# Performance work log

Measured on AMD Instinct MI355X. Metric: run time of the kernel, lower is better.

Reference implementation:

```python
import jax, jax.numpy as jnp
import numpy as np

H = 16  # n_heads


def _ln(x, g, b, eps=1e-5):
    m = x.mean(-1, keepdims=True)
    v = ((x - m) ** 2).mean(-1, keepdims=True)
    return (x - m) / jnp.sqrt(v + eps) * g + b


def setup_inputs() -> dict:
    key = jax.random.key(0)
    ks = jax.random.split(key, 10)
    b, lq, d, dff, L = 2, 1024, 1024, 4096, 4
    s = 0.02
    return {
        "x": jax.random.normal(ks[0], (b, lq, d), jnp.float32),
        "memory_bank": jax.random.normal(ks[1], (L, b, lq, d), jnp.float32),
        "attn_mask": jax.random.bernoulli(ks[2], 0.3, (b, lq, lq)),
        "ln1_g": jnp.ones((d,), jnp.float32),
        "ln1_b": jnp.zeros((d,), jnp.float32),
        "Wq": jax.random.normal(ks[3], (d, d), jnp.float32) * s,
        "Wk": jax.random.normal(ks[4], (d, d), jnp.float32) * s,
        "Wv": jax.random.normal(ks[5], (d, d), jnp.float32) * s,
        "Wo": jax.random.normal(ks[6], (d, d), jnp.float32) * s,
        "ln2_g": jnp.ones((d,), jnp.float32),
        "ln2_b": jnp.zeros((d,), jnp.float32),
        "W1": jax.random.normal(ks[7], (d, dff), jnp.float32) * s,
        "b1": jnp.zeros((dff,), jnp.float32),
        "W2": jax.random.normal(ks[8], (dff, d), jnp.float32) * s,
        "b2": jnp.zeros((d,), jnp.float32),
    }


def reference(x, memory_bank, attn_mask, ln1_g, ln1_b, Wq, Wk, Wv, Wo,
              ln2_g, ln2_b, W1, b1, W2, b2):
    # x: [b, lq, d]; memory_bank: [L, b, lk, d]; attn_mask: [b, lq, lk] bool (True = masked)
    b, lq, d = x.shape
    dh = d // H
    # preprocess_attn: LayerNorm (eval mode -> dropouts are identity)
    q = _ln(x, ln1_g, ln1_b)
    # grow memory bank with current normalized input
    mem = jnp.concatenate([memory_bank, q[None]], axis=0)  # [L+1, b, lk, d]
    L, _, lk, _ = mem.shape
    # projections (bias-free); key/value projected per layer then flattened over (L, lk)
    pq = (q @ Wq).reshape(b, lq, H, dh).transpose(0, 2, 1, 3) * (dh ** -0.5)  # [b,h,lq,dh]
    pk = (mem @ Wk).transpose(1, 0, 2, 3).reshape(b, L * lk, H, dh).transpose(0, 2, 1, 3)
    pv = (mem @ Wv).transpose(1, 0, 2, 3).reshape(b, L * lk, H, dh).transpose(0, 2, 1, 3)
    scores = jnp.einsum('bhqd,bhkd->bhqk', pq, pk)           # [b,h,lq,L*lk]
    scores = scores.reshape(b, H, lq, L, lk)
    scores = jnp.where(attn_mask[:, None, :, None, :], -jnp.inf, scores)
    attn = jax.nn.softmax(scores.reshape(b, H, lq, L * lk), axis=-1)
    ctx = jnp.einsum('bhqk,bhkd->bhqd', attn, pv)            # [b,h,lq,dh]
    ctx = ctx.transpose(0, 2, 1, 3).reshape(b, lq, d)
    attn_out = ctx @ Wo
    # postprocess_attn: residual add
    x2 = x + attn_out
    # FFN: LayerNorm -> Linear -> ReLU -> Linear -> residual
    f = _ln(x2, ln2_g, ln2_b)
    f = jax.nn.relu(f @ W1 + b1) @ W2 + b2
    out = x2 + f
    return (out, mem)
```

## Files before the change

### kernel.cpp

```cpp
#include <hip/hip_runtime.h>
#include <hip/hip_bf16.h>

typedef __attribute__((ext_vector_type(8))) __bf16 bf16x8;
typedef __attribute__((ext_vector_type(4))) __bf16 bf16x4;
typedef __attribute__((ext_vector_type(4))) float f32x4;
typedef __attribute__((ext_vector_type(16))) float f32x16;

#define MFMA16(a, b, c) __builtin_amdgcn_mfma_f32_16x16x32_bf16((a), (b), (c), 0, 0, 0)
#define MFMA32(a, b, c) __builtin_amdgcn_mfma_f32_32x32x16_bf16((a), (b), (c), 0, 0, 0)
#define LOG2E 1.4426950408889634f

static __device__ __forceinline__ float exp2_fast(float x) {
    float r; asm("v_exp_f32 %0, %1" : "=v"(r) : "v"(x)); return r;
}

__device__ __forceinline__ void gll16(const void* g, void* l) {
    __builtin_amdgcn_global_load_lds((const __attribute__((address_space(1))) void*)g,
                                     (__attribute__((address_space(3))) void*)l,
                                     16, 0, 0);
}

__global__ __launch_bounds__(256) void prep_kernel(const float* __restrict__ bank,
                                                   float* __restrict__ mem_out,
                                                   __bf16* __restrict__ membf,
                                                   const float* __restrict__ x,
                                                   const float* __restrict__ g,
                                                   const float* __restrict__ bta,
                                                   float* __restrict__ q_out,
                                                   __bf16* __restrict__ qbf) {
    __shared__ float rs[4], rs2[4];
    int blk = blockIdx.x;
    if (blk < 2048) {
        int i = blk * 256 + threadIdx.x;
        const float4* i4 = (const float4*)bank;
        float4* o4 = (float4*)mem_out;
        for (; i < 2097152; i += 2048 * 256) {
            float4 v = i4[i];
            o4[i] = v;
            if (membf) {
                bf16x4 ob = {(__bf16)v.x, (__bf16)v.y, (__bf16)v.z, (__bf16)v.w};
                ((bf16x4*)membf)[i] = ob;
            }
        }
    } else {
        int row = blk - 2048;
        const float4 v = ((const float4*)(x + (size_t)row * 1024))[threadIdx.x];
        float s = v.x + v.y + v.z + v.w;
        float s2 = v.x * v.x + v.y * v.y + v.z * v.z + v.w * v.w;
#pragma unroll
        for (int off = 1; off < 64; off <<= 1) {
            s += __shfl_xor(s, off);
            s2 += __shfl_xor(s2, off);
        }
        int wv = threadIdx.x >> 6;
        if ((threadIdx.x & 63) == 0) { rs[wv] = s; rs2[wv] = s2; }
        __syncthreads();
        s = rs[0] + rs[1] + rs[2] + rs[3];
        s2 = rs2[0] + rs2[1] + rs2[2] + rs2[3];
        float mean = s * (1.0f / 1024.0f);
        float var = s2 * (1.0f / 1024.0f) - mean * mean;
        float rstd = rsqrtf(var + 1e-5f);
        float4 gg = ((const float4*)g)[threadIdx.x];
        float4 bb = ((const float4*)bta)[threadIdx.x];
        float4 o;
        o.x = (v.x - mean) * rstd * gg.x + bb.x;
        o.y = (v.y - mean) * rstd * gg.y + bb.y;
        o.z = (v.z - mean) * rstd * gg.z + bb.z;
        o.w = (v.w - mean) * rstd * gg.w + bb.w;
        ((float4*)(q_out + (size_t)row * 1024))[threadIdx.x] = o;
        if (qbf) {
            bf16x4 ob = {(__bf16)o.x, (__bf16)o.y, (__bf16)o.z, (__bf16)o.w};
            ((bf16x4*)(qbf + (size_t)row * 1024))[threadIdx.x] = ob;
        }
    }
}

__global__ __launch_bounds__(256) void ln_kernel(const float* __restrict__ x,
                                                 const float* __restrict__ g,
                                                 const float* __restrict__ bta,
                                                 __bf16* __restrict__ outb) {
    int row = blockIdx.x;
    const float4 v = ((const float4*)(x + (size_t)row * 1024))[threadIdx.x];
    float s = v.x + v.y + v.z + v.w;
    float s2 = v.x * v.x + v.y * v.y + v.z * v.z + v.w * v.w;
#pragma unroll
    for (int off = 1; off < 64; off <<= 1) {
        s += __shfl_xor(s, off);
        s2 += __shfl_xor(s2, off);
    }
    __shared__ float rs[4], rs2[4];
    int wv = threadIdx.x >> 6;
    if ((threadIdx.x & 63) == 0) { rs[wv] = s; rs2[wv] = s2; }
    __syncthreads();
    s = rs[0] + rs[1] + rs[2] + rs[3];
    s2 = rs2[0] + rs2[1] + rs2[2] + rs2[3];
    float mean = s * (1.0f / 1024.0f);
    float var = s2 * (1.0f / 1024.0f) - mean * mean;
    float rstd = rsqrtf(var + 1e-5f);
    float4 gg = ((const float4*)g)[threadIdx.x];
    float4 bb = ((const float4*)bta)[threadIdx.x];
    bf16x4 ob;
    ob[0] = (__bf16)((v.x - mean) * rstd * gg.x + bb.x);
    ob[1] = (__bf16)((v.y - mean) * rstd * gg.y + bb.y);
    ob[2] = (__bf16)((v.z - mean) * rstd * gg.z + bb.z);
    ob[3] = (__bf16)((v.w - mean) * rstd * gg.w + bb.w);
    ((bf16x4*)(outb + (size_t)row * 1024))[threadIdx.x] = ob;
}

__global__ __launch_bounds__(256) void comb_ln2(const float* __restrict__ pc0,
                                                const float* __restrict__ pc1,
                                                const float* __restrict__ x,
                                                const float* __restrict__ g,
                                                const float* __restrict__ bta,
                                                float* __restrict__ x2,
                                                __bf16* __restrict__ fln) {
    int row = blockIdx.x;
    int idx = row * 256 + threadIdx.x;
    float4 a = ((const float4*)pc0)[idx];
    float4 b = ((const float4*)pc1)[idx];
    float4 r = ((const float4*)x)[idx];
    float4 v;
    v.x = a.x + b.x + r.x;
    v.y = a.y + b.y + r.y;
    v.z = a.z + b.z + r.z;
    v.w = a.w + b.w + r.w;
    ((float4*)x2)[idx] = v;
    float s = v.x + v.y + v.z + v.w;
    float s2 = v.x * v.x + v.y * v.y + v.z * v.z + v.w * v.w;
#pragma unroll
    for (int off = 1; off < 64; off <<= 1) {
        s += __shfl_xor(s, off);
        s2 += __shfl_xor(s2, off);
    }
    __shared__ float rs[4], rs2[4];
    int wv = threadIdx.x >> 6;
    if ((threadIdx.x & 63) == 0) { rs[wv] = s; rs2[wv] = s2; }
    __syncthreads();
    s = rs[0] + rs[1] + rs[2] + rs[3];
    s2 = rs2[0] + rs2[1] + rs2[2] + rs2[3];
    float mean = s * (1.0f / 1024.0f);
    float var = s2 * (1.0f / 1024.0f) - mean * mean;
    float rstd = rsqrtf(var + 1e-5f);
    float4 gg = ((const float4*)g)[threadIdx.x];
    float4 bb = ((const float4*)bta)[threadIdx.x];
    bf16x4 ob;
    ob[0] = (__bf16)((v.x - mean) * rstd * gg.x + bb.x);
    ob[1] = (__bf16)((v.y - mean) * rstd * gg.y + bb.y);
    ob[2] = (__bf16)((v.z - mean) * rstd * gg.z + bb.z);
    ob[3] = (__bf16)((v.w - mean) * rstd * gg.w + bb.w);
    ((bf16x4*)(fln + (size_t)row * 1024))[threadIdx.x] = ob;
}

__device__ __forceinline__ void tr_body(const float* __restrict__ in, __bf16* __restrict__ out,
                                        int K, int N, int k0, int n0) {
    __shared__ float tile[32][33];
    int tx = threadIdx.x & 31, ty = threadIdx.x >> 5;
#pragma unroll
    for (int i = 0; i < 4; i++)
        tile[ty + i * 8][tx] = in[(size_t)(k0 + ty + i * 8) * N + n0 + tx];
    __syncthreads();
#pragma unroll
    for (int i = 0; i < 4; i++)
        out[(size_t)(n0 + ty + i * 8) * K + k0 + tx] = (__bf16)tile[tx][ty + i * 8];
}

__global__ __launch_bounds__(256) void tr_early(const float* __restrict__ Wq,
                                                const float* __restrict__ Wk,
                                                const float* __restrict__ Wv,
                                                __bf16* __restrict__ Wq_t,
                                                __bf16* __restrict__ Wkv_t) {
    int w = blockIdx.x;
    int sel = w >> 10, within = w & 1023;
    const float* in = (sel == 0) ? Wq : ((sel == 1) ? Wk : Wv);
    __bf16* out = (sel == 0) ? Wq_t : (Wkv_t + (size_t)(sel - 1) * 1048576);
    tr_body(in, out, 1024, 1024, (within >> 5) * 32, (within & 31) * 32);
}

__global__ __launch_bounds__(256) void tr_late(const float* __restrict__ Wo,
                                               const float* __restrict__ W1,
                                               const float* __restrict__ W2,
                                               __bf16* __restrict__ Wo_t,
                                               __bf16* __restrict__ W1_t,
                                               __bf16* __restrict__ W2_t) {
    int w = blockIdx.x;
    const float* in;
    __bf16* out;
    int K, N, k0, n0;
    if (w < 1024) {
        in = Wo; out = Wo_t; K = 1024; N = 1024; n0 = (w & 31) * 32; k0 = (w >> 5) * 32;
    } else if (w < 5120) {
        int v = w - 1024;
        in = W1; out = W1_t; K = 1024; N = 4096; n0 = (v & 127) * 32; k0 = (v >> 7) * 32;
    } else {
        int v = w - 5120;
        in = W2; out = W2_t; K = 4096; N = 1024; n0 = (v & 31) * 32; k0 = (v >> 5) * 32;
    }
    tr_body(in, out, K, N, k0, n0);
}

template <int EPI, bool ABF16>
__device__ __forceinline__ void gemm_core(const void* __restrict__ Av,
                                          const __bf16* __restrict__ Bt,
                                          void* __restrict__ Cout,
                                          const float* __restrict__ bias,
                                          const float* __restrict__ res,
                                          int N, int lda, int ldb, int klen,
                                          float scale, int bm, int bn) {
    constexpr int LDA = ABF16 ? 32 : 40;
    __shared__ __bf16 As[128 * LDA];
    __shared__ __bf16 Bs[128 * 32];

    int t = threadIdx.x;
    int lane = t & 63, wave = t >> 6;
    int wm = (wave >> 1) * 64, wn = (wave & 1) * 64;
    int l16 = lane & 15, l4 = lane >> 4;

    f32x4 acc[4][4];
#pragma unroll
    for (int m = 0; m < 4; m++)
#pragma unroll
        for (int n = 0; n < 4; n++) acc[m][n] = (f32x4){0.f, 0.f, 0.f, 0.f};

    int srow = t >> 2;
    int scol = (t & 3) * 8;
    int ar = t >> 1, ak = (t & 1) * 16;
    const __bf16* Ab = (const __bf16*)Av;
    const float* Af = (const float*)Av;

    for (int k0 = 0; k0 < klen; k0 += 32) {
        gll16(Bt + (size_t)(bn + srow) * ldb + (k0 + scol), &Bs[wave * 512]);
        gll16(Bt + (size_t)(bn + 64 + srow) * ldb + (k0 + scol), &Bs[2048 + wave * 512]);
        if constexpr (ABF16) {
            gll16(Ab + (size_t)(bm + srow) * lda + (k0 + scol), &As[wave * 512]);
            gll16(Ab + (size_t)(bm + 64 + srow) * lda + (k0 + scol), &As[2048 + wave * 512]);
        } else {
            const float* ap = Af + (size_t)(bm + ar) * lda + k0 + ak;
            float4 f0 = ((const float4*)ap)[0];
            float4 f1 = ((const float4*)ap)[1];
            float4 f2 = ((const float4*)ap)[2];
            float4 f3 = ((const float4*)ap)[3];
            float ta[16] = {f0.x, f0.y, f0.z, f0.w, f1.x, f1.y, f1.z, f1.w,
                            f2.x, f2.y, f2.z, f2.w, f3.x, f3.y, f3.z, f3.w};
            bf16x8 v0, v1;
#pragma unroll
            for (int j = 0; j < 8; j++) { v0[j] = (__bf16)ta[j]; v1[j] = (__bf16)ta[j + 8]; }
            *(bf16x8*)&As[ar * 40 + ak] = v0;
            *(bf16x8*)&As[ar * 40 + ak + 8] = v1;
        }
        __syncthreads();

        bf16x8 af[4], bfr[4];
#pragma unroll
        for (int m = 0; m < 4; m++) af[m] = *(const bf16x8*)&As[(wm + m * 16 + l16) * LDA + l4 * 8];
#pragma unroll
        for (int n = 0; n < 4; n++) bfr[n] = *(const bf16x8*)&Bs[(wn + n * 16 + l16) * 32 + l4 * 8];
#pragma unroll
        for (int m = 0; m < 4; m++)
#pragma unroll
            for (int n = 0; n < 4; n++) acc[m][n] = MFMA16(af[m], bfr[n], acc[m][n]);
        __syncthreads();
    }

#pragma unroll
    for (int m = 0; m < 4; m++) {
#pragma unroll
        for (int r = 0; r < 4; r++) {
            int row = bm + wm + m * 16 + l4 * 4 + r;
#pragma unroll
            for (int n = 0; n < 4; n++) {
                int col = bn + wn + n * 16 + l16;
                float c = acc[m][n][r];
                size_t idx = (size_t)row * N + col;
                if (EPI == 0) {
                    ((__bf16*)Cout)[idx] = (__bf16)(c * scale);
                } else if (EPI == 1) {
                    ((float*)Cout)[idx] = c + res[idx];
                } else if (EPI == 2) {
                    ((__bf16*)Cout)[idx] = (__bf16)fmaxf(c + bias[col], 0.0f);
                } else if (EPI == 3) {
                    ((float*)Cout)[idx] = c + bias[col] + res[idx];
                } else {
                    ((float*)Cout)[idx] = c;
                }
            }
        }
    }
}

template <int EPI, bool ABF16>
__global__ __launch_bounds__(256) void gemm_bt(const void* __restrict__ Av,
                                               const __bf16* __restrict__ Bt,
                                               void* __restrict__ Cout,
                                               const float* __restrict__ bias,
                                               const float* __restrict__ res,
                                               int N, int K, float scale, int nbx) {
    int q = gridDim.x >> 3;
    int swz = (blockIdx.x & 7) * q + (blockIdx.x >> 3);
    int bn = (swz % nbx) * 128;
    int bm = (swz / nbx) * 128;
    gemm_core<EPI, ABF16>(Av, Bt, Cout, bias, res, N, K, K, K, scale, bm, bn);
}

template <bool ABF16>
__global__ __launch_bounds__(256) void gemm_proj(const void* __restrict__ Akv,
                                                 const __bf16* __restrict__ Wkv_t,
                                                 __bf16* __restrict__ PKV,
                                                 const void* __restrict__ Aq,
                                                 const __bf16* __restrict__ Wq_t,
                                                 __bf16* __restrict__ Pq) {
    int q = gridDim.x >> 3;
    int swz = (blockIdx.x & 7) * q + (blockIdx.x >> 3);
    const void* A;
    const __bf16* B;
    __bf16* C;
    int N, bm, bn;
    float sc;
    if (swz < 1280) {
        A = Akv; B = Wkv_t; C = PKV; N = 2048; sc = 1.0f;
        bn = (swz & 15) * 128; bm = (swz >> 4) * 128;
    } else {
        int p = swz - 1280;
        A = Aq; B = Wq_t; C = Pq; N = 1024; sc = 0.125f * LOG2E;
        bn = (p & 7) * 128; bm = (p >> 3) * 128;
    }
    gemm_core<0, ABF16>(A, B, C, nullptr, nullptr, N, 1024, 1024, 1024, sc, bm, bn);
}

__global__ __launch_bounds__(256) void gemm_w2(const __bf16* __restrict__ h1,
                                               const __bf16* __restrict__ W2_t,
                                               float* __restrict__ pc0,
                                               float* __restrict__ pc1) {
    int q = gridDim.x >> 3;
    int swz = (blockIdx.x & 7) * q + (blockIdx.x >> 3);
    int half = swz >> 7;
    int p = swz & 127;
    int bn = (p & 7) * 128, bm = (p >> 3) * 128;
    int koff = half * 2048;
    gemm_core<4, true>(h1 + koff, W2_t + koff, half ? pc1 : pc0, nullptr, nullptr,
                       1024, 4096, 4096, 2048, 1.0f, bm, bn);
}

__global__ __launch_bounds__(256) void gemm_wo(const __bf16* __restrict__ ctx,
                                               const __bf16* __restrict__ Wo_t,
                                               float* __restrict__ pc0,
                                               float* __restrict__ pc1) {
    int q = gridDim.x >> 3;
    int swz = (blockIdx.x & 7) * q + (blockIdx.x >> 3);
    int half = swz >> 7;
    int p = swz & 127;
    int bn = (p & 7) * 128, bm = (p >> 3) * 128;
    int koff = half * 512;
    gemm_core<4, true>(ctx + koff, Wo_t + koff, half ? pc1 : pc0, nullptr, nullptr,
                       1024, 1024, 1024, 512, 1.0f, bm, bn);
}

__global__ __launch_bounds__(256) void comb_kernel(const float* __restrict__ pc0,
                                                   const float* __restrict__ pc1,
                                                   const float* __restrict__ bias,
                                                   const float* __restrict__ res,
                                                   float* __restrict__ out) {
    int i = blockIdx.x * 256 + threadIdx.x;
    float4 a = ((const float4*)pc0)[i];
    float4 b = ((const float4*)pc1)[i];
    float4 r = ((const float4*)res)[i];
    float4 o;
    o.x = a.x + b.x + r.x;
    o.y = a.y + b.y + r.y;
    o.z = a.z + b.z + r.z;
    o.w = a.w + b.w + r.w;
    if (bias) {
        float4 bb = ((const float4*)bias)[i & 255];
        o.x += bb.x; o.y += bb.y; o.z += bb.z; o.w += bb.w;
    }
    ((float4*)out)[i] = o;
}

__global__ __launch_bounds__(256, 3) void attn_part(const __bf16* __restrict__ Pq,
                                                    const __bf16* __restrict__ PKV,
                                                    const unsigned char* __restrict__ mask,
                                                    __bf16* __restrict__ pacc,
                                                    float* __restrict__ pl) {
    int bh = blockIdx.x;
    int b = bh >> 4, h = bh & 15;
    int rng = blockIdx.z;
    int wave = threadIdx.x >> 6, lane = threadIdx.x & 63;
    int l32 = lane & 31, hi = lane >> 5;
    int q0 = blockIdx.y * 128 + wave * 32;

    __shared__ __bf16 Ks[64][64];
    __shared__ __bf16 Vt[64][64];
    __shared__ __bf16 Ps[4][32][64];

    bf16x8 qf[4];
    {
        const __bf16* pqrow = Pq + (size_t)(b * 1024 + q0 + l32) * 1024 + h * 64 + hi * 8;
#pragma unroll
        for (int ds = 0; ds < 4; ds++) qf[ds] = *(const bf16x8*)(pqrow + ds * 16);
    }

    f32x16 acc0, acc1;
#pragma unroll
    for (int i = 0; i < 16; i++) { acc0[i] = 0.f; acc1[i] = 0.f; }
    float lsum = 0.0f;

    const unsigned char* mrow_p = mask + (size_t)b * (1024u * 1024u)
                                  + (size_t)(q0 + l32) * 1024 + hi * 4;

    int tl = threadIdx.x;
    int skey = tl >> 2;
    int sd0 = (tl & 3) << 4;
    int kgbase = rng * 1280;

    int Gq = (l32 ^ (l32 >> 3)) & 7;
    int Gk = (skey ^ (skey >> 3)) & 7;
    int kw0 = skey * 64 + ((((sd0 >> 3) + 0) ^ Gk) << 3);
    int kw1 = skey * 64 + ((((sd0 >> 3) + 1) ^ Gk) << 3);
    int vwa[16];
#pragma unroll
    for (int j = 0; j < 16; j++) {
        int row = sd0 + j;
        int Gr = (row ^ (row >> 3)) & 7;
        vwa[j] = row * 64 + ((((skey >> 3) ^ Gr) << 3) | (skey & 7));
    }
    __bf16* KsF = &Ks[0][0];
    __bf16* VtF = &Vt[0][0];
    __bf16* PsF = &Ps[wave][0][0];

    bf16x8 rk0, rk1, rv0, rv1;
    unsigned int mk[8], mkn[8];
    {
        int kg = kgbase + skey;
        int lidx = kg >> 10, i = kg & 1023;
        size_t off = ((size_t)(lidx * 2048 + b * 1024 + i) << 11) + h * 64 + sd0;
        rk0 = *(const bf16x8*)(PKV + off);
        rk1 = *(const bf16x8*)(PKV + off + 8);
        rv0 = *(const bf16x8*)(PKV + off + 1024);
        rv1 = *(const bf16x8*)(PKV + off + 1032);
        int kloc = kgbase & 1023;
#pragma unroll
        for (int d = 0; d < 8; d++)
            mk[d] = *(const unsigned int*)(mrow_p + kloc + (d >> 2) * 32 + (d & 3) * 8);
    }

    for (int t = 0; t < 20; t++) {
        *(bf16x8*)&KsF[kw0] = rk0;
        *(bf16x8*)&KsF[kw1] = rk1;
#pragma unroll
        for (int j = 0; j < 8; j++) { VtF[vwa[j]] = rv0[j]; VtF[vwa[j + 8]] = rv1[j]; }
        __syncthreads();

        if (t + 1 < 20) {
            int kg = kgbase + (t + 1) * 64 + skey;
            int lidx = kg >> 10, i = kg & 1023;
            size_t off = ((size_t)(lidx * 2048 + b * 1024 + i) << 11) + h * 64 + sd0;
            rk0 = *(const bf16x8*)(PKV + off);
            rk1 = *(const bf16x8*)(PKV + off + 8);
            rv0 = *(const bf16x8*)(PKV + off + 1024);
            rv1 = *(const bf16x8*)(PKV + off + 1032);
            int kloc = (kgbase + (t + 1) * 64) & 1023;
#pragma unroll
            for (int d = 0; d < 8; d++)
                mkn[d] = *(const unsigned int*)(mrow_p + kloc + (d >> 2) * 32 + (d & 3) * 8);
        }

        float psum = 0.0f;
#pragma unroll
        for (int kb = 0; kb < 2; kb++) {
            f32x16 s;
#pragma unroll
            for (int i = 0; i < 16; i++) s[i] = 0.f;
            __builtin_amdgcn_s_setprio(1);
#pragma unroll
            for (int ds = 0; ds < 4; ds++) {
                int row = kb * 32 + l32;
                int Gr = (row ^ (row >> 3)) & 7;
                bf16x8 ka = *(const bf16x8*)&KsF[row * 64 + (((ds * 2 + hi) ^ Gr) << 3)];
                s = MFMA32(ka, qf[ds], s);
            }
            __builtin_amdgcn_s_setprio(0);
#pragma unroll
            for (int g = 0; g < 4; g++) {
                bf16x4 pk_;
                unsigned int mkd = mk[kb * 4 + g];
#pragma unroll
                for (int m = 0; m < 4; m++) {
                    float e = exp2_fast(s[g * 4 + m]);
                    e = ((mkd >> (m * 8)) & 255u) ? 0.0f : e;
                    psum += e;
                    pk_[m] = (__bf16)e;
                }
                *(bf16x4*)&PsF[l32 * 64 + ((((kb * 4 + g) ^ Gq) << 3) | (hi * 4))] = pk_;
            }
        }
        lsum += psum;
#pragma unroll
        for (int d = 0; d < 8; d++) mk[d] = mkn[d];

        __builtin_amdgcn_s_setprio(1);
#pragma unroll
        for (int ks = 0; ks < 4; ks++) {
            bf16x8 pf = *(const bf16x8*)&PsF[l32 * 64 + (((ks * 2 + hi) ^ Gq) << 3)];
            {
                int row = l32;
                int Gr = (row ^ (row >> 3)) & 7;
                bf16x8 vf = *(const bf16x8*)&VtF[row * 64 + (((ks * 2 + hi) ^ Gr) << 3)];
                acc0 = MFMA32(vf, pf, acc0);
            }
            {
                int row = 32 + l32;
                int Gr = (row ^ (row >> 3)) & 7;
                bf16x8 vf = *(const bf16x8*)&VtF[row * 64 + (((ks * 2 + hi) ^ Gr) << 3)];
                acc1 = MFMA32(vf, pf, acc1);
            }
        }
        __builtin_amdgcn_s_setprio(0);
        __syncthreads();
    }

    lsum += __shfl_xor(lsum, 32);

    size_t blk = ((size_t)(bh * 8 + blockIdx.y) * 4 + rng);
    __bf16* pa = pacc + blk * 8192 + (size_t)(wave * 32 + l32) * 64;
#pragma unroll
    for (int g = 0; g < 4; g++) {
        bf16x4 o0, o1;
#pragma unroll
        for (int m = 0; m < 4; m++) {
            o0[m] = (__bf16)acc0[g * 4 + m];
            o1[m] = (__bf16)acc1[g * 4 + m];
        }
        *(bf16x4*)&pa[g * 8 + hi * 4] = o0;
        *(bf16x4*)&pa[32 + g * 8 + hi * 4] = o1;
    }
    if (hi == 0) pl[blk * 128 + wave * 32 + l32] = lsum;
}

__global__ __launch_bounds__(512) void attn_comb(const __bf16* __restrict__ pacc,
                                                 const float* __restrict__ pl,
                                                 __bf16* __restrict__ ctx) {
    int bh = blockIdx.x, qb = blockIdx.y;
    int b = bh >> 4, h = bh & 15;
    int q = threadIdx.x >> 2, d0 = (threadIdx.x & 3) * 16;
    float acc[16];
#pragma unroll
    for (int j = 0; j < 16; j++) acc[j] = 0.0f;
    float l = 0.0f;
    size_t blk0 = ((size_t)(bh * 8 + qb)) * 4;
#pragma unroll
    for (int rng = 0; rng < 4; rng++) {
        size_t base = (blk0 + rng) * 8192 + (size_t)q * 64 + d0;
        bf16x8 a0 = *(const bf16x8*)&pacc[base];
        bf16x8 a1 = *(const bf16x8*)&pacc[base + 8];
#pragma unroll
        for (int j = 0; j < 8; j++) {
            acc[j] += (float)a0[j];
            acc[8 + j] += (float)a1[j];
        }
        l += pl[(blk0 + rng) * 128 + q];
    }
    float inv = 1.0f / l;
    __bf16* crow = ctx + ((size_t)(b * 1024 + qb * 128 + q) << 10) + h * 64 + d0;
    bf16x8 o0, o1;
#pragma unroll
    for (int j = 0; j < 8; j++) {
        o0[j] = (__bf16)(acc[j] * inv);
        o1[j] = (__bf16)(acc[8 + j] * inv);
    }
    *(bf16x8*)crow = o0;
    *(bf16x8*)(crow + 8) = o1;
}

#define KHALF 2560
#define CK 64
#define NCH 40
__global__ __launch_bounds__(512, 4) void attn_kernel(const __bf16* __restrict__ Pq,
                                                      const __bf16* __restrict__ PKV,
                                                      const unsigned char* __restrict__ mask,
                                                      __bf16* __restrict__ ctx) {
    int bh = blockIdx.x;
    int b = bh >> 4, h = bh & 15;
    int wave = threadIdx.x >> 6, lane = threadIdx.x & 63;
    int grp = wave >> 2, wv = wave & 3;
    int l16 = lane & 15, l4 = lane >> 4;
    int q0 = blockIdx.y * 64 + wv * 16;

    __shared__ __bf16 Ks[2][64][72];
    __shared__ __bf16 Vt[2][64][72];
    __shared__ __bf16 Ps[8][16][72];

    const f32x4 fzero = {0.f, 0.f, 0.f, 0.f};

    bf16x8 qf[2];
    {
        const __bf16* pqrow = Pq + (size_t)(b * 1024 + q0 + l16) * 1024 + h * 64;
        qf[0] = *(const bf16x8*)(pqrow + l4 * 8);
        qf[1] = *(const bf16x8*)(pqrow + 32 + l4 * 8);
    }

    f32x4 accT[4];
#pragma unroll
    for (int n = 0; n < 4; n++) accT[n] = fzero;
    float lsum = 0.0f;

    const unsigned char* mrow_p = mask + (size_t)b * (1024u * 1024u) + (size_t)(q0 + l16) * 1024;

    int tl = threadIdx.x & 255;
    int skey = tl >> 2;
    int sd0 = (tl & 3) << 4;
    int kgbase = grp * KHALF;

    bf16x8 rk0, rk1, rv0, rv1;
    unsigned int mk[4], mkn[4];
    {
        int kg = kgbase + skey;
        int lidx = kg >> 10, i = kg & 1023;
        size_t off = ((size_t)(lidx * 2048 + b * 1024 + i) << 11) + h * 64 + sd0;
        rk0 = *(const bf16x8*)(PKV + off);
        rk1 = *(const bf16x8*)(PKV + off + 8);
        rv0 = *(const bf16x8*)(PKV + off + 1024);
        rv1 = *(const bf16x8*)(PKV + off + 1032);
        int kloc = kgbase & 1023;
#pragma unroll
        for (int tile = 0; tile < 4; tile++)
            mk[tile] = *(const unsigned int*)(mrow_p + kloc + tile * 16 + l4 * 4);
    }

    for (int t = 0; t < NCH; t++) {
        *(bf16x8*)&Ks[grp][skey][sd0] = rk0;
        *(bf16x8*)&Ks[grp][skey][sd0 + 8] = rk1;
#pragma unroll
        for (int j = 0; j < 8; j++) {
            int row = sd0 + j;
            Vt[grp][row][skey ^ ((row >> 3) << 3)] = rv0[j];
            int row2 = sd0 + 8 + j;
            Vt[grp][row2][skey ^ ((row2 >> 3) << 3)] = rv1[j];
        }
        __syncthreads();

        if (t + 1 < NCH) {
            int kg = kgbase + (t + 1) * CK + skey;
            int lidx = kg >> 10, i = kg & 1023;
            size_t off = ((size_t)(lidx * 2048 + b * 1024 + i) << 11) + h * 64 + sd0;
            rk0 = *(const bf16x8*)(PKV + off);
            rk1 = *(const bf16x8*)(PKV + off + 8);
            rv0 = *(const bf16x8*)(PKV + off + 1024);
            rv1 = *(const bf16x8*)(PKV + off + 1032);
            int kloc = (kgbase + (t + 1) * CK) & 1023;
#pragma unroll
            for (int tile = 0; tile < 4; tile++)
                mkn[tile] = *(const unsigned int*)(mrow_p + kloc + tile * 16 + l4 * 4);
        }

        f32x4 s[4];
        __builtin_amdgcn_s_setprio(1);
#pragma unroll
        for (int tile = 0; tile < 4; tile++) {
            bf16x8 ka = *(const bf16x8*)&Ks[grp][tile * 16 + l16][l4 * 8];
            bf16x8 kb = *(const bf16x8*)&Ks[grp][tile * 16 + l16][32 + l4 * 8];
            f32x4 sz = fzero;
            sz = MFMA16(ka, qf[0], sz);
            sz = MFMA16(kb, qf[1], sz);
            s[tile] = sz;
        }
        __builtin_amdgcn_s_setprio(0);

        float psum = 0.0f;
#pragma unroll
        for (int tile = 0; tile < 4; tile++) {
            bf16x4 pk_;
#pragma unroll
            for (int r = 0; r < 4; r++) {
                float e = exp2_fast(s[tile][r]);
                e = ((mk[tile] >> (r * 8)) & 255u) ? 0.0f : e;
                psum += e;
                pk_[r] = (__bf16)e;
            }
            *(bf16x4*)&Ps[wave][l16][tile * 16 + l4 * 4] = pk_;
        }
        lsum += psum;
#pragma unroll
        for (int tile = 0; tile < 4; tile++) mk[tile] = mkn[tile];

        __builtin_amdgcn_s_setprio(1);
#pragma unroll
        for (int kk = 0; kk < 2; kk++) {
            bf16x8 pf = *(const bf16x8*)&Ps[wave][l16][kk * 32 + l4 * 8];
#pragma unroll
            for (int n = 0; n < 4; n++) {
                int row = n * 16 + l16;
                int colblk = (kk * 32 + l4 * 8) ^ ((row >> 3) << 3);
                bf16x8 vf = *(const bf16x8*)&Vt[grp][row][colblk];
                accT[n] = MFMA16(vf, pf, accT[n]);
            }
        }
        __builtin_amdgcn_s_setprio(0);
        __syncthreads();
    }

    lsum += __shfl_xor(lsum, 16);
    lsum += __shfl_xor(lsum, 32);

    float* exAcc = (float*)&Ks[0][0][0];
    float* exL = (float*)&Vt[0][0][0];
    if (grp == 1) {
#pragma unroll
        for (int n = 0; n < 4; n++)
            *(f32x4*)&exAcc[(wv * 16 + l16) * 68 + n * 16 + l4 * 4] = accT[n];
        if (l4 == 0) exL[wv * 16 + l16] = lsum;
    }
    __syncthreads();
    if (grp == 0) {
        int qi = wv * 16 + l16;
        float inv = 1.0f / (lsum + exL[qi]);
        __bf16* crow = ctx + ((size_t)(b * 1024 + q0 + l16) << 10) + h * 64;
#pragma unroll
        for (int n = 0; n < 4; n++) {
            f32x4 a1 = *(const f32x4*)&exAcc[qi * 68 + n * 16 + l4 * 4];
            bf16x4 o;
#pragma unroll
            for (int r = 0; r < 4; r++) o[r] = (__bf16)((accT[n][r] + a1[r]) * inv);
            *(bf16x4*)&crow[n * 16 + l4 * 4] = o;
        }
    }
}

extern "C" void kernel_launch(void* const* d_in, const int* in_sizes, int n_in,
                              void* d_out, int out_size, void* d_ws, size_t ws_size,
                              hipStream_t stream) {
    const float* x = (const float*)d_in[0];
    const float* memory_bank = (const float*)d_in[1];
    const unsigned char* attn_mask = (const unsigned char*)d_in[2];
    const float* ln1_g = (const float*)d_in[3];
    const float* ln1_b = (const float*)d_in[4];
    const float* Wq = (const float*)d_in[5];
    const float* Wk = (const float*)d_in[6];
    const float* Wv = (const float*)d_in[7];
    const float* Wo = (const float*)d_in[8];
    const float* ln2_g = (const float*)d_in[9];
    const float* ln2_b = (const float*)d_in[10];
    const float* W1 = (const float*)d_in[11];
    const float* b1 = (const float*)d_in[12];
    const float* W2 = (const float*)d_in[13];
    const float* b2 = (const float*)d_in[14];

    float* out = (float*)d_out;
    float* mem_out = out + 2097152;
    float* q_out = mem_out + 4 * 2097152;

    char* ws = (char*)d_ws;
    bool big = ws_size >= (70ull << 20);

    __bf16* PKV = (__bf16*)ws;
    __bf16 *Pq, *Wq_t, *Wkv_t, *ctx, *membf = nullptr, *qbf = nullptr;
    __bf16* pacc = nullptr;
    float* plv = nullptr;
    if (big) {
        membf = (__bf16*)(ws + (40ull << 20));
        qbf = membf + (size_t)8192 * 1024;
        Wq_t = (__bf16*)(ws + (60ull << 20));
        Wkv_t = (__bf16*)(ws + (62ull << 20));
        Pq = (__bf16*)(ws + (66ull << 20));
        ctx = (__bf16*)(ws + (60ull << 20));
        pacc = (__bf16*)(ws + (40ull << 20));
        plv = (float*)(ws + (56ull << 20));
    } else {
        Pq = (__bf16*)(ws + (40ull << 20));
        Wq_t = (__bf16*)(ws + (44ull << 20));
        Wkv_t = (__bf16*)(ws + (46ull << 20));
        ctx = (__bf16*)(ws + (44ull << 20));
    }
    __bf16* Wo_t = (__bf16*)ws;
    __bf16* W1_t = (__bf16*)(ws + (2ull << 20));
    __bf16* W2_t = (__bf16*)(ws + (10ull << 20));
    float* x2 = (float*)(ws + (18ull << 20));
    __bf16* fln = (__bf16*)(ws + (26ull << 20));
    __bf16* h1 = (__bf16*)(ws + (30ull << 20));
    float* wo_pc0 = (float*)(ws + (30ull << 20));
    float* wo_pc1 = (float*)(ws + (38ull << 20));
    float* pc0 = (float*)(ws + (46ull << 20));
    float* pc1 = (float*)(ws + (54ull << 20));

    prep_kernel<<<4096, 256, 0, stream>>>(memory_bank, mem_out, membf, x, ln1_g, ln1_b,
                                          q_out, qbf);
    tr_early<<<3072, 256, 0, stream>>>(Wq, Wk, Wv, Wq_t, Wkv_t);

    if (big)
        gemm_proj<true><<<1408, 256, 0, stream>>>(membf, Wkv_t, PKV, qbf, Wq_t, Pq);
    else
        gemm_proj<false><<<1408, 256, 0, stream>>>(mem_out, Wkv_t, PKV, q_out, Wq_t, Pq);

    if (big) {
        attn_part<<<dim3(32, 8, 4), 256, 0, stream>>>(Pq, PKV, attn_mask, pacc, plv);
        attn_comb<<<dim3(32, 8), 512, 0, stream>>>(pacc, plv, ctx);
    } else {
        attn_kernel<<<dim3(32, 16), 512, 0, stream>>>(Pq, PKV, attn_mask, ctx);
    }

    tr_late<<<9216, 256, 0, stream>>>(Wo, W1, W2, Wo_t, W1_t, W2_t);

    if (big) {
        gemm_wo<<<256, 256, 0, stream>>>(ctx, Wo_t, wo_pc0, wo_pc1);
        comb_ln2<<<2048, 256, 0, stream>>>(wo_pc0, wo_pc1, x, ln2_g, ln2_b, x2, fln);
    } else {
        gemm_bt<1, true><<<128, 256, 0, stream>>>(ctx, Wo_t, x2, nullptr, x, 1024, 1024, 1.0f, 8);
        ln_kernel<<<2048, 256, 0, stream>>>(x2, ln2_g, ln2_b, fln);
    }
    gemm_bt<2, true><<<512, 256, 0, stream>>>(fln, W1_t, h1, b1, nullptr, 4096, 1024, 1.0f, 32);
    if (big) {
        gemm_w2<<<256, 256, 0, stream>>>(h1, W2_t, pc0, pc1);
        comb_kernel<<<2048, 256, 0, stream>>>(pc0, pc1, b2, x2, out);
    } else {
        gemm_bt<3, true><<<128, 256, 0, stream>>>(h1, W2_t, out, b2, x2, 1024, 4096, 1.0f, 8);
    }
}
```

Before: 293.4 us.

## Bit-pack attention mask and double-buffer split-K attention with 64-query waves

```diff
diff --git a/kernel.cpp b/kernel.cpp
--- a/kernel.cpp
+++ b/kernel.cpp
@@ -27,7 +27,9 @@
                                                    const float* __restrict__ g,
                                                    const float* __restrict__ bta,
                                                    float* __restrict__ q_out,
-                                                   __bf16* __restrict__ qbf) {
+                                                   __bf16* __restrict__ qbf,
+                                                   const unsigned char* __restrict__ mask,
+                                                   unsigned int* __restrict__ mbits) {
     __shared__ float rs[4], rs2[4];
     int blk = blockIdx.x;
     if (blk < 2048) {
@@ -42,7 +44,7 @@
                 ((bf16x4*)membf)[i] = ob;
             }
         }
-    } else {
+    } else if (blk < 4096) {
         int row = blk - 2048;
         const float4 v = ((const float4*)(x + (size_t)row * 1024))[threadIdx.x];
         float s = v.x + v.y + v.z + v.w;
@@ -71,6 +73,17 @@
         if (qbf) {
             bf16x4 ob = {(__bf16)o.x, (__bf16)o.y, (__bf16)o.z, (__bf16)o.w};
             ((bf16x4*)(qbf + (size_t)row * 1024))[threadIdx.x] = ob;
+        }
+    } else if (mbits) {
+        int row = blk - 4096;
+        const unsigned char* mrow = mask + (size_t)row * 1024;
+        int w = threadIdx.x >> 6, l = threadIdx.x & 63;
+        unsigned long long* dst = (unsigned long long*)(mbits + (size_t)row * 32);
+#pragma unroll
+        for (int i = 0; i < 4; i++) {
+            int key = i * 256 + w * 64 + l;
+            unsigned long long bal = __ballot(mrow[key] != 0);
+            if (l == 0) dst[i * 4 + w] = bal;
         }
     }
 }
@@ -375,9 +388,44 @@
     ((float4*)out)[i] = o;
 }
 
-__global__ __launch_bounds__(256, 3) void attn_part(const __bf16* __restrict__ Pq,
+__device__ __forceinline__ void softmax_p(const f32x16& s0, const f32x16& s1,
+                                          unsigned int mka, unsigned int mkb,
+                                          int hi, float& lsum, bf16x8* pf) {
+    unsigned int ow[8][2];
+#pragma unroll
+    for (int g = 0; g < 4; g++) {
+        bf16x4 p0, p1;
+#pragma unroll
+        for (int m = 0; m < 4; m++) {
+            float e = exp2_fast(s0[g * 4 + m]);
+            e = ((mka >> (g * 8 + hi * 4 + m)) & 1u) ? 0.0f : e;
+            lsum += e;
+            p0[m] = (__bf16)e;
+            float e2 = exp2_fast(s1[g * 4 + m]);
+            e2 = ((mkb >> (g * 8 + hi * 4 + m)) & 1u) ? 0.0f : e2;
+            lsum += e2;
+            p1[m] = (__bf16)e2;
+        }
+        ow[g][0] = ((unsigned int*)&p0)[0];
+        ow[g][1] = ((unsigned int*)&p0)[1];
+        ow[4 + g][0] = ((unsigned int*)&p1)[0];
+        ow[4 + g][1] = ((unsigned int*)&p1)[1];
+    }
+#pragma unroll
+    for (int ks = 0; ks < 4; ks++) {
+        unsigned int a0 = ow[2 * ks][0], b0 = ow[2 * ks + 1][0];
+        unsigned int a1 = ow[2 * ks][1], b1 = ow[2 * ks + 1][1];
+        asm volatile("v_permlane32_swap_b32 %0, %1" : "+v"(a0), "+v"(b0));
+        asm volatile("v_permlane32_swap_b32 %0, %1" : "+v"(a1), "+v"(b1));
+        unsigned int* pp = (unsigned int*)&pf[ks];
+        pp[0] = a0; pp[1] = a1; pp[2] = b0; pp[3] = b1;
+    }
+}
+
+#define NCHP 20
+__global__ __launch_bounds__(256, 2) void attn_part(const __bf16* __restrict__ Pq,
                                                     const __bf16* __restrict__ PKV,
-                                                    const unsigned char* __restrict__ mask,
+                                                    const unsigned int* __restrict__ mbits,
                                                     __bf16* __restrict__ pacc,
                                                     float* __restrict__ pl) {
     int bh = blockIdx.x;
@@ -385,33 +433,31 @@
     int rng = blockIdx.z;
     int wave = threadIdx.x >> 6, lane = threadIdx.x & 63;
     int l32 = lane & 31, hi = lane >> 5;
-    int q0 = blockIdx.y * 128 + wave * 32;
-
-    __shared__ __bf16 Ks[64][64];
-    __shared__ __bf16 Vt[64][64];
-    __shared__ __bf16 Ps[4][32][64];
-
-    bf16x8 qf[4];
-    {
-        const __bf16* pqrow = Pq + (size_t)(b * 1024 + q0 + l32) * 1024 + h * 64 + hi * 8;
-#pragma unroll
-        for (int ds = 0; ds < 4; ds++) qf[ds] = *(const bf16x8*)(pqrow + ds * 16);
-    }
-
-    f32x16 acc0, acc1;
-#pragma unroll
-    for (int i = 0; i < 16; i++) { acc0[i] = 0.f; acc1[i] = 0.f; }
-    float lsum = 0.0f;
-
-    const unsigned char* mrow_p = mask + (size_t)b * (1024u * 1024u)
-                                  + (size_t)(q0 + l32) * 1024 + hi * 4;
+    int q0 = blockIdx.y * 256 + wave * 64;
+
+    __shared__ __bf16 Ks[2][64][64];
+    __shared__ __bf16 Vt[2][64][64];
+
+    bf16x8 qf[2][4];
+#pragma unroll
+    for (int tile = 0; tile < 2; tile++) {
+        const __bf16* pqrow = Pq + (size_t)(b * 1024 + q0 + tile * 32 + l32) * 1024 + h * 64 + hi * 8;
+#pragma unroll
+        for (int ds = 0; ds < 4; ds++) qf[tile][ds] = *(const bf16x8*)(pqrow + ds * 16);
+    }
+
+    f32x16 acc00, acc01, acc10, acc11;
+#pragma unroll
+    for (int i = 0; i < 16; i++) { acc00[i] = 0.f; acc01[i] = 0.f; acc10[i] = 0.f; acc11[i] = 0.f; }
+    float lsum0 = 0.0f, lsum1 = 0.0f;
+
+    const unsigned int* mrow0 = mbits + (size_t)(b * 1024 + q0 + l32) * 32;
+    const unsigned int* mrow1 = mbits + (size_t)(b * 1024 + q0 + 32 + l32) * 32;
 
     int tl = threadIdx.x;
-    int skey = tl >> 2;
-    int sd0 = (tl & 3) << 4;
+    int skey = tl >> 2, sd0 = (tl & 3) << 4;
     int kgbase = rng * 1280;
 
-    int Gq = (l32 ^ (l32 >> 3)) & 7;
     int Gk = (skey ^ (skey >> 3)) & 7;
     int kw0 = skey * 64 + ((((sd0 >> 3) + 0) ^ Gk) << 3);
     int kw1 = skey * 64 + ((((sd0 >> 3) + 1) ^ Gk) << 3);
@@ -422,12 +468,15 @@
         int Gr = (row ^ (row >> 3)) & 7;
         vwa[j] = row * 64 + ((((skey >> 3) ^ Gr) << 3) | (skey & 7));
     }
-    __bf16* KsF = &Ks[0][0];
-    __bf16* VtF = &Vt[0][0];
-    __bf16* PsF = &Ps[wave][0][0];
+    __bf16* KsF = &Ks[0][0][0];
+    __bf16* VtF = &Vt[0][0][0];
+
+    int Gr0 = (l32 ^ (l32 >> 3)) & 7;
+    int r1v = 32 + l32;
+    int Gr1 = (r1v ^ (r1v >> 3)) & 7;
 
     bf16x8 rk0, rk1, rv0, rv1;
-    unsigned int mk[8], mkn[8];
+
     {
         int kg = kgbase + skey;
         int lidx = kg >> 10, i = kg & 1023;
@@ -436,103 +485,109 @@
         rk1 = *(const bf16x8*)(PKV + off + 8);
         rv0 = *(const bf16x8*)(PKV + off + 1024);
         rv1 = *(const bf16x8*)(PKV + off + 1032);
-        int kloc = kgbase & 1023;
-#pragma unroll
-        for (int d = 0; d < 8; d++)
-            mk[d] = *(const unsigned int*)(mrow_p + kloc + (d >> 2) * 32 + (d & 3) * 8);
-    }
-
-    for (int t = 0; t < 20; t++) {
-        *(bf16x8*)&KsF[kw0] = rk0;
-        *(bf16x8*)&KsF[kw1] = rk1;
-#pragma unroll
-        for (int j = 0; j < 8; j++) { VtF[vwa[j]] = rv0[j]; VtF[vwa[j + 8]] = rv1[j]; }
+    }
+    *(bf16x8*)&KsF[kw0] = rk0;
+    *(bf16x8*)&KsF[kw1] = rk1;
+#pragma unroll
+    for (int j = 0; j < 8; j++) { VtF[vwa[j]] = rv0[j]; VtF[vwa[j + 8]] = rv1[j]; }
+    {
+        int kg = kgbase + 64 + skey;
+        int lidx = kg >> 10, i = kg & 1023;
+        size_t off = ((size_t)(lidx * 2048 + b * 1024 + i) << 11) + h * 64 + sd0;
+        rk0 = *(const bf16x8*)(PKV + off);
+        rk1 = *(const bf16x8*)(PKV + off + 8);
+        rv0 = *(const bf16x8*)(PKV + off + 1024);
+        rv1 = *(const bf16x8*)(PKV + off + 1032);
+    }
+    int kd0 = (kgbase & 1023) >> 5;
+    unsigned int mk0a = mrow0[kd0], mk0b = mrow0[kd0 + 1];
+    unsigned int mk1a = mrow1[kd0], mk1b = mrow1[kd0 + 1];
+
+    for (int t = 0; t < NCHP; t++) {
+        int cbo = (t & 1) << 12;
+        int nbo = cbo ^ 4096;
         __syncthreads();
-
-        if (t + 1 < 20) {
-            int kg = kgbase + (t + 1) * 64 + skey;
+        if (t + 1 < NCHP) {
+            *(bf16x8*)&KsF[nbo + kw0] = rk0;
+            *(bf16x8*)&KsF[nbo + kw1] = rk1;
+#pragma unroll
+            for (int j = 0; j < 8; j++) { VtF[nbo + vwa[j]] = rv0[j]; VtF[nbo + vwa[j + 8]] = rv1[j]; }
+        }
+        if (t + 2 < NCHP) {
+            int kg = kgbase + (t + 2) * 64 + skey;
             int lidx = kg >> 10, i = kg & 1023;
             size_t off = ((size_t)(lidx * 2048 + b * 1024 + i) << 11) + h * 64 + sd0;
             rk0 = *(const bf16x8*)(PKV + off);
             rk1 = *(const bf16x8*)(PKV + off + 8);
             rv0 = *(const bf16x8*)(PKV + off + 1024);
             rv1 = *(const bf16x8*)(PKV + off + 1032);
-            int kloc = (kgbase + (t + 1) * 64) & 1023;
-#pragma unroll
-            for (int d = 0; d < 8; d++)
-                mkn[d] = *(const unsigned int*)(mrow_p + kloc + (d >> 2) * 32 + (d & 3) * 8);
-        }
-
-        float psum = 0.0f;
-#pragma unroll
-        for (int kb = 0; kb < 2; kb++) {
-            f32x16 s;
-#pragma unroll
-            for (int i = 0; i < 16; i++) s[i] = 0.f;
-            __builtin_amdgcn_s_setprio(1);
-#pragma unroll
-            for (int ds = 0; ds < 4; ds++) {
-                int row = kb * 32 + l32;
-                int Gr = (row ^ (row >> 3)) & 7;
-                bf16x8 ka = *(const bf16x8*)&KsF[row * 64 + (((ds * 2 + hi) ^ Gr) << 3)];
-                s = MFMA32(ka, qf[ds], s);
-            }
-            __builtin_amdgcn_s_setprio(0);
-#pragma unroll
-            for (int g = 0; g < 4; g++) {
-                bf16x4 pk_;
-                unsigned int mkd = mk[kb * 4 + g];
-#pragma unroll
-                for (int m = 0; m < 4; m++) {
-                    float e = exp2_fast(s[g * 4 + m]);
-                    e = ((mkd >> (m * 8)) & 255u) ? 0.0f : e;
-                    psum += e;
-                    pk_[m] = (__bf16)e;
-                }
-                *(bf16x4*)&PsF[l32 * 64 + ((((kb * 4 + g) ^ Gq) << 3) | (hi * 4))] = pk_;
-            }
-        }
-        lsum += psum;
-#pragma unroll
-        for (int d = 0; d < 8; d++) mk[d] = mkn[d];
-
+        }
+        unsigned int nk0a = 0, nk0b = 0, nk1a = 0, nk1b = 0;
+        if (t + 1 < NCHP) {
+            int kdn = ((kgbase + (t + 1) * 64) & 1023) >> 5;
+            nk0a = mrow0[kdn]; nk0b = mrow0[kdn + 1];
+            nk1a = mrow1[kdn]; nk1b = mrow1[kdn + 1];
+        }
+
+        f32x16 s00, s01, s10, s11;
+#pragma unroll
+        for (int i = 0; i < 16; i++) { s00[i] = 0.f; s01[i] = 0.f; s10[i] = 0.f; s11[i] = 0.f; }
         __builtin_amdgcn_s_setprio(1);
 #pragma unroll
+        for (int ds = 0; ds < 4; ds++) {
+            bf16x8 ka0 = *(const bf16x8*)&KsF[cbo + l32 * 64 + (((ds * 2 + hi) ^ Gr0) << 3)];
+            bf16x8 ka1 = *(const bf16x8*)&KsF[cbo + r1v * 64 + (((ds * 2 + hi) ^ Gr1) << 3)];
+            s00 = MFMA32(ka0, qf[0][ds], s00);
+            s10 = MFMA32(ka0, qf[1][ds], s10);
+            s01 = MFMA32(ka1, qf[0][ds], s01);
+            s11 = MFMA32(ka1, qf[1][ds], s11);
+        }
+        __builtin_amdgcn_s_setprio(0);
+
+        bf16x8 pf0[4], pf1[4];
+        softmax_p(s00, s01, mk0a, mk0b, hi, lsum0, pf0);
+        softmax_p(s10, s11, mk1a, mk1b, hi, lsum1, pf1);
+
+        mk0a = nk0a; mk0b = nk0b; mk1a = nk1a; mk1b = nk1b;
+
+        __builtin_amdgcn_s_setprio(1);
+#pragma unroll
         for (int ks = 0; ks < 4; ks++) {
-            bf16x8 pf = *(const bf16x8*)&PsF[l32 * 64 + (((ks * 2 + hi) ^ Gq) << 3)];
-            {
-                int row = l32;
-                int Gr = (row ^ (row >> 3)) & 7;
-                bf16x8 vf = *(const bf16x8*)&VtF[row * 64 + (((ks * 2 + hi) ^ Gr) << 3)];
-                acc0 = MFMA32(vf, pf, acc0);
-            }
-            {
-                int row = 32 + l32;
-                int Gr = (row ^ (row >> 3)) & 7;
-                bf16x8 vf = *(const bf16x8*)&VtF[row * 64 + (((ks * 2 + hi) ^ Gr) << 3)];
-                acc1 = MFMA32(vf, pf, acc1);
-            }
+            bf16x8 vf0 = *(const bf16x8*)&VtF[cbo + l32 * 64 + (((ks * 2 + hi) ^ Gr0) << 3)];
+            bf16x8 vf1 = *(const bf16x8*)&VtF[cbo + r1v * 64 + (((ks * 2 + hi) ^ Gr1) << 3)];
+            acc00 = MFMA32(vf0, pf0[ks], acc00);
+            acc01 = MFMA32(vf1, pf0[ks], acc01);
+            acc10 = MFMA32(vf0, pf1[ks], acc10);
+            acc11 = MFMA32(vf1, pf1[ks], acc11);
         }
         __builtin_amdgcn_s_setprio(0);
-        __syncthreads();
-    }
-
-    lsum += __shfl_xor(lsum, 32);
-
-    size_t blk = ((size_t)(bh * 8 + blockIdx.y) * 4 + rng);
-    __bf16* pa = pacc + blk * 8192 + (size_t)(wave * 32 + l32) * 64;
+    }
+
+    lsum0 += __shfl_xor(lsum0, 32);
+    lsum1 += __shfl_xor(lsum1, 32);
+
+    size_t blk = ((size_t)(bh * 4 + blockIdx.y) * 4 + rng);
+    __bf16* pa0 = pacc + blk * 16384 + (size_t)(wave * 64 + l32) * 64;
+    __bf16* pa1 = pacc + blk * 16384 + (size_t)(wave * 64 + 32 + l32) * 64;
 #pragma unroll
     for (int g = 0; g < 4; g++) {
-        bf16x4 o0, o1;
+        bf16x4 o00, o01, o10, o11;
 #pragma unroll
         for (int m = 0; m < 4; m++) {
-            o0[m] = (__bf16)acc0[g * 4 + m];
-            o1[m] = (__bf16)acc1[g * 4 + m];
-        }
-        *(bf16x4*)&pa[g * 8 + hi * 4] = o0;
-        *(bf16x4*)&pa[32 + g * 8 + hi * 4] = o1;
-    }
-    if (hi == 0) pl[blk * 128 + wave * 32 + l32] = lsum;
+            o00[m] = (__bf16)acc00[g * 4 + m];
+            o01[m] = (__bf16)acc01[g * 4 + m];
+            o10[m] = (__bf16)acc10[g * 4 + m];
+            o11[m] = (__bf16)acc11[g * 4 + m];
+        }
+        *(bf16x4*)&pa0[g * 8 + hi * 4] = o00;
+        *(bf16x4*)&pa0[32 + g * 8 + hi * 4] = o01;
+        *(bf16x4*)&pa1[g * 8 + hi * 4] = o10;
+        *(bf16x4*)&pa1[32 + g * 8 + hi * 4] = o11;
+    }
+    if (hi == 0) {
+        pl[blk * 256 + wave * 64 + l32] = lsum0;
+        pl[blk * 256 + wave * 64 + 32 + l32] = lsum1;
+    }
 }
 
 __global__ __launch_bounds__(512) void attn_comb(const __bf16* __restrict__ pacc,
@@ -540,34 +595,32 @@
                                                  __bf16* __restrict__ ctx) {
     int bh = blockIdx.x, qb = blockIdx.y;
     int b = bh >> 4, h = bh & 15;
-    int q = threadIdx.x >> 2, d0 = (threadIdx.x & 3) * 16;
-    float acc[16];
-#pragma unroll
-    for (int j = 0; j < 16; j++) acc[j] = 0.0f;
+    int q = threadIdx.x >> 1, dhalf = (threadIdx.x & 1) * 32;
+    float acc[32];
+#pragma unroll
+    for (int j = 0; j < 32; j++) acc[j] = 0.0f;
     float l = 0.0f;
-    size_t blk0 = ((size_t)(bh * 8 + qb)) * 4;
+    size_t blk0 = ((size_t)(bh * 4 + qb)) * 4;
 #pragma unroll
     for (int rng = 0; rng < 4; rng++) {
-        size_t base = (blk0 + rng) * 8192 + (size_t)q * 64 + d0;
-        bf16x8 a0 = *(const bf16x8*)&pacc[base];
-        bf16x8 a1 = *(const bf16x8*)&pacc[base + 8];
-#pragma unroll
-        for (int j = 0; j < 8; j++) {
-            acc[j] += (float)a0[j];
-            acc[8 + j] += (float)a1[j];
-        }
-        l += pl[(blk0 + rng) * 128 + q];
+        size_t base = (blk0 + rng) * 16384 + (size_t)q * 64 + dhalf;
+#pragma unroll
+        for (int v = 0; v < 4; v++) {
+            bf16x8 a = *(const bf16x8*)&pacc[base + v * 8];
+#pragma unroll
+            for (int j = 0; j < 8; j++) acc[v * 8 + j] += (float)a[j];
+        }
+        l += pl[(blk0 + rng) * 256 + q];
     }
     float inv = 1.0f / l;
-    __bf16* crow = ctx + ((size_t)(b * 1024 + qb * 128 + q) << 10) + h * 64 + d0;
-    bf16x8 o0, o1;
-#pragma unroll
-    for (int j = 0; j < 8; j++) {
-        o0[j] = (__bf16)(acc[j] * inv);
-        o1[j] = (__bf16)(acc[8 + j] * inv);
-    }
-    *(bf16x8*)crow = o0;
-    *(bf16x8*)(crow + 8) = o1;
+    __bf16* crow = ctx + ((size_t)(b * 1024 + qb * 256 + q) << 10) + h * 64 + dhalf;
+#pragma unroll
+    for (int v = 0; v < 4; v++) {
+        bf16x8 o;
+#pragma unroll
+        for (int j = 0; j < 8; j++) o[j] = (__bf16)(acc[v * 8 + j] * inv);
+        *(bf16x8*)&crow[v * 8] = o;
+    }
 }
 
 #define KHALF 2560
@@ -754,6 +807,7 @@
     __bf16 *Pq, *Wq_t, *Wkv_t, *ctx, *membf = nullptr, *qbf = nullptr;
     __bf16* pacc = nullptr;
     float* plv = nullptr;
+    unsigned int* mbits = nullptr;
     if (big) {
         membf = (__bf16*)(ws + (40ull << 20));
         qbf = membf + (size_t)8192 * 1024;
@@ -763,6 +817,7 @@
         ctx = (__bf16*)(ws + (60ull << 20));
         pacc = (__bf16*)(ws + (40ull << 20));
         plv = (float*)(ws + (56ull << 20));
+        mbits = (unsigned int*)(ws + (30ull << 20));
     } else {
         Pq = (__bf16*)(ws + (40ull << 20));
         Wq_t = (__bf16*)(ws + (44ull << 20));
@@ -780,8 +835,8 @@
     float* pc0 = (float*)(ws + (46ull << 20));
     float* pc1 = (float*)(ws + (54ull << 20));
 
-    prep_kernel<<<4096, 256, 0, stream>>>(memory_bank, mem_out, membf, x, ln1_g, ln1_b,
-                                          q_out, qbf);
+    prep_kernel<<<6144, 256, 0, stream>>>(memory_bank, mem_out, membf, x, ln1_g, ln1_b,
+                                          q_out, qbf, attn_mask, mbits);
     tr_early<<<3072, 256, 0, stream>>>(Wq, Wk, Wv, Wq_t, Wkv_t);
 
     if (big)
@@ -790,8 +845,8 @@
         gemm_proj<false><<<1408, 256, 0, stream>>>(mem_out, Wkv_t, PKV, q_out, Wq_t, Pq);
 
     if (big) {
-        attn_part<<<dim3(32, 8, 4), 256, 0, stream>>>(Pq, PKV, attn_mask, pacc, plv);
-        attn_comb<<<dim3(32, 8), 512, 0, stream>>>(pacc, plv, ctx);
+        attn_part<<<dim3(32, 4, 4), 256, 0, stream>>>(Pq, PKV, mbits, pacc, plv);
+        attn_comb<<<dim3(32, 4), 512, 0, stream>>>(pacc, plv, ctx);
     } else {
         attn_kernel<<<dim3(32, 16), 512, 0, stream>>>(Pq, PKV, attn_mask, ctx);
     }
```

Result: faster. 271.7 us (-7.4%).
